# Kernel optimization log

Hardware: AMD Instinct MI355X
Metric: run time of the kernel (lower is better)

The kernel has to match this reference:

```python
import jax, jax.numpy as jnp
import numpy as np

SCALES = (4, 8, 8)
PAD = 2
TOTAL = 256  # prod(SCALES) == frame shift
INDENT = PAD * TOTAL
BN_EPS = 1e-3  # keras BatchNormalization default


def _bn(x, g, b, m, v):
    return (x - m) * jax.lax.rsqrt(v + BN_EPS) * g + b


def _conv1d_valid(x, w):
    # x: [B, T, Cin], w: [K, Cin, Cout]
    return jax.lax.conv_general_dilated(x, w, (1,), 'VALID',
                                         dimension_numbers=('NWC', 'WIO', 'NWC'))


def _mel_conv_same(x, w):
    # per-mel-bin shared 1D conv along time. x: [B, T, M], w: [K]
    B, T, M = x.shape
    lhs = x.transpose(0, 2, 1).reshape(B * M, T, 1)
    rhs = w.reshape(-1, 1, 1)
    y = jax.lax.conv_general_dilated(lhs, rhs, (1,), 'SAME',
                                     dimension_numbers=('NWC', 'WIO', 'NWC'))
    return y.reshape(B, M, T).transpose(0, 2, 1)


def _gru(x, Wx, Wh, bx, bh):
    # keras GRUCell (reset_after=True): gate order z, r, h; h' = z*h + (1-z)*hh
    xp = x @ Wx + bx  # [B, T, 3H], input projection hoisted out of the scan
    H = Wh.shape[0]
    h0 = jnp.zeros((x.shape[0], H), x.dtype)

    def step(h, xt):
        rp = h @ Wh + bh
        xz, xr, xh = jnp.split(xt, 3, axis=-1)
        rz, rr, rh = jnp.split(rp, 3, axis=-1)
        z = jax.nn.sigmoid(xz + rz)
        r = jax.nn.sigmoid(xr + rr)
        hh = jnp.tanh(xh + r * rh)
        hn = z * h + (1.0 - z) * hh
        return hn, hn

    _, ys = jax.lax.scan(step, h0, xp.transpose(1, 0, 2))
    return ys.transpose(1, 0, 2)


def setup_inputs() -> dict:
    key = jax.random.key(0)
    ks = iter(jax.random.split(key, 64))
    B, T_MEL, M, C, H, R = 4, 44, 80, 128, 512, 10
    T_UP = TOTAL * (T_MEL - 2 * PAD)  # 10240
    s = 0.05
    d = {}
    d['audios'] = jax.random.normal(next(ks), (B, T_UP + 1), jnp.float32)
    d['mels'] = jax.random.normal(next(ks), (B, T_MEL, M), jnp.float32)
    d['w_mel0'] = jnp.full((2 * SCALES[0] + 1,), 1.0 / (2 * SCALES[0] + 1), jnp.float32)
    d['w_mel1'] = jnp.full((2 * SCALES[1] + 1,), 1.0 / (2 * SCALES[1] + 1), jnp.float32)
    d['w_mel2'] = jnp.full((2 * SCALES[2] + 1,), 1.0 / (2 * SCALES[2] + 1), jnp.float32)
    d['mr_conv0_w'] = jax.random.normal(next(ks), (5, M, C), jnp.float32) * s
    d['mr_bn0_g'] = jax.random.uniform(next(ks), (C,), jnp.float32, 0.5, 1.5)
    d['mr_bn0_b'] = jax.random.normal(next(ks), (C,), jnp.float32) * s
    d['mr_bn0_m'] = jnp.zeros((C,), jnp.float32)
    d['mr_bn0_v'] = jnp.ones((C,), jnp.float32)
    d['r_w1'] = jax.random.normal(next(ks), (R, C, C), jnp.float32) * s
    d['r_bn1_g'] = jax.random.uniform(next(ks), (R, C), jnp.float32, 0.5, 1.5)
    d['r_bn1_b'] = jax.random.normal(next(ks), (R, C), jnp.float32) * s
    d['r_bn1_m'] = jnp.zeros((R, C), jnp.float32)
    d['r_bn1_v'] = jnp.ones((R, C), jnp.float32)
    d['r_w2'] = jax.random.normal(next(ks), (R, C, C), jnp.float32) * s
    d['r_bn2_g'] = jax.random.uniform(next(ks), (R, C), jnp.float32, 0.5, 1.5)
    d['r_bn2_b'] = jax.random.normal(next(ks), (R, C), jnp.float32) * s
    d['r_bn2_m'] = jnp.zeros((R, C), jnp.float32)
    d['r_bn2_v'] = jnp.ones((R, C), jnp.float32)
    d['mr_out_w'] = jax.random.normal(next(ks), (C, C), jnp.float32) * s
    d['mr_out_b'] = jnp.zeros((C,), jnp.float32)
    A4 = C // 4  # 32
    d['Wi'] = jax.random.normal(next(ks), (1 + M + A4, H), jnp.float32) * s
    d['bi'] = jnp.zeros((H,), jnp.float32)
    d['Wx0'] = jax.random.normal(next(ks), (H, 3 * H), jnp.float32) * s
    d['Wh0'] = jax.random.normal(next(ks), (H, 3 * H), jnp.float32) * s
    d['bx0'] = jnp.zeros((3 * H,), jnp.float32)
    d['bh0'] = jnp.zeros((3 * H,), jnp.float32)
    d['Wx1'] = jax.random.normal(next(ks), (H + A4, 3 * H), jnp.float32) * s
    d['Wh1'] = jax.random.normal(next(ks), (H, 3 * H), jnp.float32) * s
    d['bx1'] = jnp.zeros((3 * H,), jnp.float32)
    d['bh1'] = jnp.zeros((3 * H,), jnp.float32)
    d['Wd0'] = jax.random.normal(next(ks), (H + A4, H), jnp.float32) * s
    d['bd0'] = jnp.zeros((H,), jnp.float32)
    d['Wd1'] = jax.random.normal(next(ks), (H + A4, H), jnp.float32) * s
    d['bd1'] = jnp.zeros((H,), jnp.float32)
    d['Wp'] = jax.random.normal(next(ks), (H, 30), jnp.float32) * s
    d['bp'] = jnp.zeros((30,), jnp.float32)
    return d


def reference(audios, mels, w_mel0, w_mel1, w_mel2,
              mr_conv0_w, mr_bn0_g, mr_bn0_b, mr_bn0_m, mr_bn0_v,
              r_w1, r_bn1_g, r_bn1_b, r_bn1_m, r_bn1_v,
              r_w2, r_bn2_g, r_bn2_b, r_bn2_m, r_bn2_v,
              mr_out_w, mr_out_b, Wi, bi,
              Wx0, Wh0, bx0, bh0, Wx1, Wh1, bx1, bh1,
              Wd0, bd0, Wd1, bd1, Wp, bp):
    # ---- UpsampleNet mel branch: nearest upsample + smoothing conv per scale ----
    x = mels
    for w, scale in zip((w_mel0, w_mel1, w_mel2), SCALES):
        x = jnp.repeat(x, scale, axis=1)
        x = _mel_conv_same(x, w)
    mels_up = x[:, INDENT:-INDENT, :]  # [B, T_up, 80]

    # ---- UpsampleNet aux branch: MelResNet (inference BN) + nearest upsample ----
    a = jax.nn.relu(_bn(_conv1d_valid(mels, mr_conv0_w),
                        mr_bn0_g, mr_bn0_b, mr_bn0_m, mr_bn0_v))
    for i in range(r_w1.shape[0]):
        y = jax.nn.relu(_bn(a @ r_w1[i], r_bn1_g[i], r_bn1_b[i], r_bn1_m[i], r_bn1_v[i]))
        y = _bn(y @ r_w2[i], r_bn2_g[i], r_bn2_b[i], r_bn2_m[i], r_bn2_v[i])
        a = a + y
    a = a @ mr_out_w + mr_out_b
    aux = jnp.repeat(a, TOTAL, axis=1)  # [B, T_up, 128]
    a0, a1, a2, a3 = jnp.split(aux, 4, axis=-1)

    # ---- WaveRNN teacher-forced trunk ----
    x = jnp.concatenate([audios[:, :-1, None], mels_up, a0], axis=-1)
    x = x @ Wi + bi  # [B, T_up, 512]
    x = _gru(x, Wx0, Wh0, bx0, bh0) + x
    x = _gru(jnp.concatenate([x, a1], axis=-1), Wx1, Wh1, bx1, bh1) + x
    x = jax.nn.relu(jnp.concatenate([x, a2], axis=-1) @ Wd0 + bd0) + x
    x = jax.nn.relu(jnp.concatenate([x, a3], axis=-1) @ Wd1 + bd1) + x
    logits = x @ Wp + bp  # [B, T_up, 30] (MoL parameters)
    return logits
```

## Files before the change

### kernel.cpp

```cpp
#include <hip/hip_runtime.h>
#include <hip/hip_bf16.h>

#define T_SEQ 10240
#define GRU_W 8

typedef short bf16x8 __attribute__((ext_vector_type(8)));
typedef float f32x4 __attribute__((ext_vector_type(4)));

__device__ __forceinline__ float bf2f(unsigned short u) {
    return __uint_as_float(((unsigned int)u) << 16);
}

__global__ void upsample_kernel(const float* __restrict__ in, float* __restrict__ out,
                                const float* __restrict__ wk,
                                int B, int Tin, int Tout, int shift, int taps)
{
    int idx = blockIdx.x * blockDim.x + threadIdx.x;
    int total = B * Tout * 80;
    if (idx >= total) return;
    int m = idx % 80;
    int r = idx / 80;
    int t = r % Tout;
    int b = r / Tout;
    int s = taps >> 1;
    float acc = 0.f;
    for (int d = -s; d <= s; ++d) {
        int i = t + d;
        if (i >= 0 && i < Tout)
            acc += in[((size_t)b * Tin + (i >> shift)) * 80 + m] * wk[d + s];
    }
    out[idx] = acc;
}

__global__ __launch_bounds__(128) void conv0_kernel(
    const float* __restrict__ mels, const float* __restrict__ w,
    const float* __restrict__ g, const float* __restrict__ b,
    const float* __restrict__ m_, const float* __restrict__ v_,
    float* __restrict__ a)
{
    __shared__ float xin[400];
    int bt = blockIdx.x;
    int bb = bt / 40, t = bt % 40;
    int c = threadIdx.x;
    for (int idx = c; idx < 400; idx += 128)
        xin[idx] = mels[((size_t)bb * 44 + t + idx / 80) * 80 + (idx % 80)];
    __syncthreads();
    float s = 0.f;
    for (int q = 0; q < 400; ++q) s += xin[q] * w[q * 128 + c];
    s = (s - m_[c]) * rsqrtf(v_[c] + 1e-3f) * g[c] + b[c];
    a[bt * 128 + c] = fmaxf(s, 0.f);
}

__global__ __launch_bounds__(128) void resblock_kernel(
    const float* __restrict__ W1, const float* __restrict__ W2,
    const float* __restrict__ g1, const float* __restrict__ b1,
    const float* __restrict__ m1, const float* __restrict__ v1,
    const float* __restrict__ g2, const float* __restrict__ b2,
    const float* __restrict__ m2, const float* __restrict__ v2,
    float* __restrict__ a)
{
    __shared__ float ain[128], y1[128];
    int tok = blockIdx.x;
    int c = threadIdx.x;
    ain[c] = a[tok * 128 + c];
    __syncthreads();
    float s = 0.f;
    #pragma unroll 8
    for (int k = 0; k < 128; ++k) s += ain[k] * W1[k * 128 + c];
    s = (s - m1[c]) * rsqrtf(v1[c] + 1e-3f) * g1[c] + b1[c];
    y1[c] = fmaxf(s, 0.f);
    __syncthreads();
    float s2 = 0.f;
    #pragma unroll 8
    for (int k = 0; k < 128; ++k) s2 += y1[k] * W2[k * 128 + c];
    s2 = (s2 - m2[c]) * rsqrtf(v2[c] + 1e-3f) * g2[c] + b2[c];
    a[tok * 128 + c] = ain[c] + s2;
}

__global__ __launch_bounds__(128) void outmat_kernel(
    const float* __restrict__ W, const float* __restrict__ bias,
    const float* __restrict__ a, float* __restrict__ out)
{
    __shared__ float ain[128];
    int tok = blockIdx.x;
    int c = threadIdx.x;
    ain[c] = a[tok * 128 + c];
    __syncthreads();
    float s = 0.f;
    #pragma unroll 8
    for (int k = 0; k < 128; ++k) s += ain[k] * W[k * 128 + c];
    out[tok * 128 + c] = s + bias[c];
}

__device__ __forceinline__ float fetchA(int mode, int row, int k, int K,
    const float* audio, const float* melsup, const float* cond, const float* xA)
{
    if (k >= K) return 0.f;
    int b = row / T_SEQ;
    int t = row - b * T_SEQ;
    if (mode == 0) {
        if (k == 0) return audio[(size_t)b * (T_SEQ + 1) + t];
        if (k < 81) return melsup[((size_t)b * 11264 + 512 + t) * 80 + (k - 1)];
        return cond[((size_t)b * 40 + (t >> 8)) * 128 + (k - 81)];
    }
    if (k < 512) return xA[(size_t)row * 512 + k];
    int co = (mode == 2) ? 32 : (mode == 3) ? 64 : 96;
    return cond[((size_t)b * 40 + (t >> 8)) * 128 + co + (k - 512)];
}

__global__ __launch_bounds__(256) void gemm_big(
    int mode, int N, int K,
    const float* __restrict__ W, const float* __restrict__ bias1,
    const float* __restrict__ bias2,
    const float* __restrict__ audio, const float* __restrict__ melsup,
    const float* __restrict__ cond, const float* __restrict__ xA,
    const float* __restrict__ resid, float* __restrict__ outF,
    __hip_bfloat16* __restrict__ outB)
{
    __shared__ float As[16][68];
    __shared__ float Bs[16][68];
    const int tid = threadIdx.x;
    const int row0 = blockIdx.y * 64;
    const int col0 = blockIdx.x * 64;
    const int tx = tid & 15, ty = tid >> 4;
    float acc[4][4] = {};
    const int nkt = (K + 15) >> 4;
    for (int kt = 0; kt < nkt; ++kt) {
        const int kb = kt << 4;
        #pragma unroll
        for (int l = 0; l < 4; ++l) {
            int k = (tid >> 6) + l * 4;
            int m = tid & 63;
            float bv = 0.f;
            if (kb + k < K) bv = W[(size_t)(kb + k) * N + col0 + m];
            Bs[k][m] = bv;
        }
        if (mode != 0) {
            int m = tid >> 2, kq = tid & 3;
            int row = row0 + m;
            int k = kb + kq * 4;
            if (k + 3 < 512) {
                float4 v = *reinterpret_cast<const float4*>(xA + (size_t)row * 512 + k);
                As[kq * 4 + 0][m] = v.x; As[kq * 4 + 1][m] = v.y;
                As[kq * 4 + 2][m] = v.z; As[kq * 4 + 3][m] = v.w;
            } else {
                #pragma unroll
                for (int i = 0; i < 4; ++i)
                    As[kq * 4 + i][m] = fetchA(mode, row, k + i, K, audio, melsup, cond, xA);
            }
        } else {
            #pragma unroll
            for (int l = 0; l < 4; ++l) {
                int k = (tid >> 6) + l * 4;
                int m = tid & 63;
                As[k][m] = fetchA(0, row0 + m, kb + k, K, audio, melsup, cond, xA);
            }
        }
        __syncthreads();
        #pragma unroll
        for (int k = 0; k < 16; ++k) {
            float a0 = As[k][(ty << 2) + 0], a1 = As[k][(ty << 2) + 1];
            float a2 = As[k][(ty << 2) + 2], a3 = As[k][(ty << 2) + 3];
            float b0 = Bs[k][(tx << 2) + 0], b1 = Bs[k][(tx << 2) + 1];
            float b2 = Bs[k][(tx << 2) + 2], b3 = Bs[k][(tx << 2) + 3];
            acc[0][0] += a0 * b0; acc[0][1] += a0 * b1; acc[0][2] += a0 * b2; acc[0][3] += a0 * b3;
            acc[1][0] += a1 * b0; acc[1][1] += a1 * b1; acc[1][2] += a1 * b2; acc[1][3] += a1 * b3;
            acc[2][0] += a2 * b0; acc[2][1] += a2 * b1; acc[2][2] += a2 * b2; acc[2][3] += a2 * b3;
            acc[3][0] += a3 * b0; acc[3][1] += a3 * b1; acc[3][2] += a3 * b2; acc[3][3] += a3 * b3;
        }
        __syncthreads();
    }
    #pragma unroll
    for (int i = 0; i < 4; ++i) {
        int row = row0 + (ty << 2) + i;
        #pragma unroll
        for (int jt = 0; jt < 4; ++jt) {
            int col = col0 + (tx << 2) + jt;
            float v = acc[i][jt] + bias1[col];
            if (bias2 && col < 1024) v += bias2[col];
            if (mode == 0) {
                outF[(size_t)row * N + col] = v;
            } else if (mode <= 2) {
                outB[(size_t)row * 1536 + col] = __float2bfloat16(v);
            } else {
                v = fmaxf(v, 0.f) + resid[(size_t)row * 512 + col];
                outF[(size_t)row * 512 + col] = v;
            }
        }
    }
}

__global__ __launch_bounds__(256) void pack_wh_kernel(const float* __restrict__ Wh,
                                                      unsigned short* __restrict__ out)
{
    int gid = blockIdx.x * 256 + threadIdx.x;
    int l = gid & 63;
    int idx = gid >> 6;
    int kt = idx & 15; idx >>= 4;
    int ntL = idx & 1; idx >>= 1;
    int w = idx % 6;
    int wg = idx / 6;
    int nt = 2 * w + ntL;
    int g = nt >> 2, u = nt & 3;
    int n = g * 512 + wg * 64 + u * 16 + (l & 15);
    int k0 = kt * 32 + (l >> 4) * 8;
    unsigned short* dst = out + (size_t)gid * 8;
    #pragma unroll
    for (int i = 0; i < 8; ++i) {
        __hip_bfloat16 hv = __float2bfloat16(Wh[(size_t)(k0 + i) * 1536 + n]);
        dst[i] = *reinterpret_cast<unsigned short*>(&hv);
    }
}

__global__ __launch_bounds__(512, 2) void gru_mfma8(
    const unsigned short* __restrict__ wpack,
    const float* __restrict__ bh,
    const __hip_bfloat16* __restrict__ xp,
    float* __restrict__ xio,
    unsigned int* __restrict__ hpair,
    int T)
{
    __shared__ alignas(16) unsigned short h_sh[16 * 512];
    __shared__ alignas(16) unsigned short xp_sh[2][4][3][64];
    __shared__ alignas(8)  float xv_sh[2][4][64];
    __shared__ alignas(16) float acc_sh[12][16][4];

    const int tid = threadIdx.x;
    const int wg = blockIdx.x;
    const int w = tid >> 6;
    const int l = tid & 63;

    {
        uint4* z = reinterpret_cast<uint4*>(h_sh);
        z[tid] = make_uint4(0, 0, 0, 0);
        z[tid + 512] = make_uint4(0, 0, 0, 0);
    }

    bf16x8 wf[2][16];
    if (w < 6) {
        const bf16x8* wp = reinterpret_cast<const bf16x8*>(wpack);
        const int base = (wg * 6 + w) * 2 * 16 * 64;
        #pragma unroll
        for (int n = 0; n < 2; ++n)
            #pragma unroll
            for (int kt = 0; kt < 16; ++kt)
                wf[n][kt] = wp[base + (n * 16 + kt) * 64 + l];
    }

    float bhh = 0.f, hprev = 0.f;
    if (tid < 256) bhh = bh[1024 + wg * 64 + (tid & 63)];

    if (tid < 128) {
        for (int z = tid; z < 192; z += 128) {
            int bg = z >> 4, s = z & 15;
            int b = bg / 3, g = bg % 3;
            unsigned long long v = *reinterpret_cast<const unsigned long long*>(
                reinterpret_cast<const unsigned short*>(xp) +
                (size_t)(b * T) * 1536 + g * 512 + wg * 64 + s * 4);
            *reinterpret_cast<unsigned long long*>(&xp_sh[0][b][g][s * 4]) = v;
        }
        int b = tid >> 5, pr = tid & 31;
        float2 v = *reinterpret_cast<const float2*>(
            xio + (size_t)(b * T) * 512 + wg * 64 + pr * 2);
        *reinterpret_cast<float2*>(&xv_sh[0][b][pr * 2]) = v;
    }
    __syncthreads();

    const unsigned long long* hp64 = reinterpret_cast<const unsigned long long*>(hpair);

    for (int t = 0; t < T; ++t) {
        const int cur = t & 1, nxt = cur ^ 1;

        const unsigned long long* src = hp64 + (size_t)cur * 1024 + tid * 2;
        const unsigned tg = (unsigned)t & 0xffffu;
        unsigned long long u0 = __hip_atomic_load(src + 0, __ATOMIC_RELAXED, __HIP_MEMORY_SCOPE_AGENT);
        unsigned long long u1 = __hip_atomic_load(src + 1, __ATOMIC_RELAXED, __HIP_MEMORY_SCOPE_AGENT);
        while ((((unsigned)(u0 >> 16) & 0xffffu) != tg) | ((unsigned)(u0 >> 48) != tg) |
               (((unsigned)(u1 >> 16) & 0xffffu) != tg) | ((unsigned)(u1 >> 48) != tg)) {
            __builtin_amdgcn_s_sleep(1);
            u0 = __hip_atomic_load(src + 0, __ATOMIC_RELAXED, __HIP_MEMORY_SCOPE_AGENT);
            u1 = __hip_atomic_load(src + 1, __ATOMIC_RELAXED, __HIP_MEMORY_SCOPE_AGENT);
        }
        {
            const int pb = tid >> 7;
            const int j0 = (tid * 4) & 511;
            unsigned long long wv =
                (u0 & 0xffffull) | ((u0 >> 32) & 0xffffull) << 16 |
                (u1 & 0xffffull) << 32 | ((u1 >> 32) & 0xffffull) << 48;
            const int chunk = (j0 >> 3) ^ (pb & 7);
            *reinterpret_cast<unsigned long long*>(
                reinterpret_cast<char*>(h_sh) + pb * 1024 + chunk * 16 + (j0 & 7) * 2) = wv;
        }
        __syncthreads();

        if (w >= 6 && t + 1 < T) {
            int t6 = tid - 384;
            for (int z = t6; z < 192; z += 128) {
                int bg = z >> 4, s = z & 15;
                int b = bg / 3, g = bg % 3;
                unsigned long long v = *reinterpret_cast<const unsigned long long*>(
                    reinterpret_cast<const unsigned short*>(xp) +
                    (size_t)(b * T + t + 1) * 1536 + g * 512 + wg * 64 + s * 4);
                *reinterpret_cast<unsigned long long*>(&xp_sh[nxt][b][g][s * 4]) = v;
            }
            int b = t6 >> 5, pr = t6 & 31;
            float2 v = *reinterpret_cast<const float2*>(
                xio + (size_t)(b * T + t + 1) * 512 + wg * 64 + pr * 2);
            *reinterpret_cast<float2*>(&xv_sh[nxt][b][pr * 2]) = v;
        }

        if (w < 6) {
            f32x4 acc0 = {0, 0, 0, 0}, acc1 = {0, 0, 0, 0};
            const int rb = l & 15, q = l >> 4;
            #pragma unroll
            for (int kt = 0; kt < 16; ++kt) {
                bf16x8 afr = *reinterpret_cast<const bf16x8*>(
                    reinterpret_cast<const char*>(h_sh) + rb * 1024 +
                    ((((kt * 4 + q) ^ (rb & 7))) << 4));
                acc0 = __builtin_amdgcn_mfma_f32_16x16x32_bf16(afr, wf[0][kt], acc0, 0, 0, 0);
                acc1 = __builtin_amdgcn_mfma_f32_16x16x32_bf16(afr, wf[1][kt], acc1, 0, 0, 0);
            }
            if (l < 16) {
                *reinterpret_cast<f32x4*>(&acc_sh[2 * w][l][0]) = acc0;
                *reinterpret_cast<f32x4*>(&acc_sh[2 * w + 1][l][0]) = acc1;
            }
        }
        __syncthreads();

        if (tid < 256) {
            const int b = tid >> 6, jl = tid & 63, j = wg * 64 + jl;
            const int u = jl >> 4, n16 = jl & 15;
            float az = acc_sh[u][n16][b];
            float ar = acc_sh[4 + u][n16][b];
            float ah = acc_sh[8 + u][n16][b];
            float xz = bf2f(xp_sh[cur][b][0][jl]);
            float xr = bf2f(xp_sh[cur][b][1][jl]);
            float xh = bf2f(xp_sh[cur][b][2][jl]);
            float xv = xv_sh[cur][b][jl];
            float z = 1.f / (1.f + __expf(-(xz + az)));
            float r = 1.f / (1.f + __expf(-(xr + ar)));
            float e2 = __expf(-2.f * (xh + r * (ah + bhh)));
            float hh = (1.f - e2) / (1.f + e2);
            float hn = z * hprev + (1.f - z) * hh;
            hprev = hn;
            __hip_bfloat16 hb16 = __float2bfloat16(hn);
            unsigned hv = ((unsigned)((t + 1) & 0xffff) << 16) |
                          (unsigned)*reinterpret_cast<unsigned short*>(&hb16);
            __hip_atomic_store(hpair + (size_t)nxt * 2048 + b * 512 + j, hv,
                               __ATOMIC_RELAXED, __HIP_MEMORY_SCOPE_AGENT);
            xio[(size_t)(b * T + t) * 512 + j] = xv + hn;
        }
    }
}

__global__ __launch_bounds__(256) void wp_kernel(
    const float* __restrict__ x, const float* __restrict__ Wp,
    const float* __restrict__ bp, float* __restrict__ out)
{
    int r = threadIdx.x >> 5, c = threadIdx.x & 31;
    size_t row = (size_t)blockIdx.x * 8 + r;
    if (c >= 30) return;
    const float* xr = x + row * 512;
    float acc = 0.f;
    #pragma unroll 8
    for (int k = 0; k < 512; ++k) acc += xr[k] * Wp[k * 30 + c];
    out[row * 30 + c] = acc + bp[c];
}

extern "C" void kernel_launch(void* const* d_in, const int* in_sizes, int n_in,
                              void* d_out, int out_size, void* d_ws, size_t ws_size,
                              hipStream_t stream)
{
    const float* audios = (const float*)d_in[0];
    const float* mels   = (const float*)d_in[1];
    const float* w_mel0 = (const float*)d_in[2];
    const float* w_mel1 = (const float*)d_in[3];
    const float* w_mel2 = (const float*)d_in[4];
    const float* conv0w = (const float*)d_in[5];
    const float* bn0g = (const float*)d_in[6];
    const float* bn0b = (const float*)d_in[7];
    const float* bn0m = (const float*)d_in[8];
    const float* bn0v = (const float*)d_in[9];
    const float* r_w1   = (const float*)d_in[10];
    const float* r_bn1g = (const float*)d_in[11];
    const float* r_bn1b = (const float*)d_in[12];
    const float* r_bn1m = (const float*)d_in[13];
    const float* r_bn1v = (const float*)d_in[14];
    const float* r_w2   = (const float*)d_in[15];
    const float* r_bn2g = (const float*)d_in[16];
    const float* r_bn2b = (const float*)d_in[17];
    const float* r_bn2m = (const float*)d_in[18];
    const float* r_bn2v = (const float*)d_in[19];
    const float* mr_out_w = (const float*)d_in[20];
    const float* mr_out_b = (const float*)d_in[21];
    const float* Wi = (const float*)d_in[22];
    const float* bi = (const float*)d_in[23];
    const float* Wx0 = (const float*)d_in[24];
    const float* Wh0 = (const float*)d_in[25];
    const float* bx0 = (const float*)d_in[26];
    const float* bh0 = (const float*)d_in[27];
    const float* Wx1 = (const float*)d_in[28];
    const float* Wh1 = (const float*)d_in[29];
    const float* bx1 = (const float*)d_in[30];
    const float* bh1 = (const float*)d_in[31];
    const float* Wd0 = (const float*)d_in[32];
    const float* bd0 = (const float*)d_in[33];
    const float* Wd1 = (const float*)d_in[34];
    const float* bd1 = (const float*)d_in[35];
    const float* Wp = (const float*)d_in[36];
    const float* bp = (const float*)d_in[37];

    char* ws = (char*)d_ws;
    size_t off = 0;
    auto alloc = [&](size_t n) { size_t r = off; off += (n + 255) & ~(size_t)255; return r; };
    const size_t M = 4 * (size_t)T_SEQ;
    size_t xp_off = alloc(M * 1536 * 2);
    size_t x_off  = alloc(M * 512 * 4);
    size_t s1_off = alloc((size_t)4 * 176 * 80 * 4);
    size_t s2_off = alloc((size_t)4 * 1408 * 80 * 4);
    size_t s3_off = alloc((size_t)4 * 11264 * 80 * 4);
    size_t ca_off = alloc((size_t)160 * 128 * 4);
    size_t cf_off = alloc((size_t)160 * 128 * 4);
    size_t wp0_off = alloc((size_t)98304 * 8 * 2);
    size_t wp1_off = alloc((size_t)98304 * 8 * 2);
    size_t hp_off  = alloc(2 * 2048 * 4);

    __hip_bfloat16* xp = (__hip_bfloat16*)(ws + xp_off);
    float* x3   = (float*)(ws + xp_off);
    float* xbuf = (float*)(ws + x_off);
    float* st1  = (float*)(ws + s1_off);
    float* st2  = (float*)(ws + s2_off);
    float* st3  = (float*)(ws + s3_off);
    float* conda = (float*)(ws + ca_off);
    float* condf = (float*)(ws + cf_off);
    unsigned short* wpack0 = (unsigned short*)(ws + wp0_off);
    unsigned short* wpack1 = (unsigned short*)(ws + wp1_off);
    unsigned int* hpair = (unsigned int*)(ws + hp_off);
    float* outp = (float*)d_out;

    pack_wh_kernel<<<384, 256, 0, stream>>>(Wh0, wpack0);
    pack_wh_kernel<<<384, 256, 0, stream>>>(Wh1, wpack1);

    {
        int tot1 = 4 * 176 * 80;
        upsample_kernel<<<(tot1 + 255) / 256, 256, 0, stream>>>(mels, st1, w_mel0, 4, 44, 176, 2, 9);
        int tot2 = 4 * 1408 * 80;
        upsample_kernel<<<(tot2 + 255) / 256, 256, 0, stream>>>(st1, st2, w_mel1, 4, 176, 1408, 3, 17);
        int tot3 = 4 * 11264 * 80;
        upsample_kernel<<<(tot3 + 255) / 256, 256, 0, stream>>>(st2, st3, w_mel2, 4, 1408, 11264, 3, 17);
    }
    conv0_kernel<<<160, 128, 0, stream>>>(mels, conv0w, bn0g, bn0b, bn0m, bn0v, conda);
    for (int i = 0; i < 10; ++i) {
        resblock_kernel<<<160, 128, 0, stream>>>(
            r_w1 + (size_t)i * 128 * 128, r_w2 + (size_t)i * 128 * 128,
            r_bn1g + i * 128, r_bn1b + i * 128, r_bn1m + i * 128, r_bn1v + i * 128,
            r_bn2g + i * 128, r_bn2b + i * 128, r_bn2m + i * 128, r_bn2v + i * 128,
            conda);
    }
    outmat_kernel<<<160, 128, 0, stream>>>(mr_out_w, mr_out_b, conda, condf);

    dim3 blk(256);
    gemm_big<<<dim3(8, 640), blk, 0, stream>>>(0, 512, 113, Wi, bi, nullptr,
        audios, st3, condf, nullptr, nullptr, xbuf, nullptr);
    gemm_big<<<dim3(24, 640), blk, 0, stream>>>(1, 1536, 512, Wx0, bx0, bh0,
        nullptr, nullptr, condf, xbuf, nullptr, nullptr, xp);
    hipMemsetAsync(ws + hp_off, 0, 2 * 2048 * 4, stream);
    gru_mfma8<<<GRU_W, 512, 0, stream>>>(wpack0, bh0, xp, xbuf, hpair, T_SEQ);
    gemm_big<<<dim3(24, 640), blk, 0, stream>>>(2, 1536, 544, Wx1, bx1, bh1,
        nullptr, nullptr, condf, xbuf, nullptr, nullptr, xp);
    hipMemsetAsync(ws + hp_off, 0, 2 * 2048 * 4, stream);
    gru_mfma8<<<GRU_W, 512, 0, stream>>>(wpack1, bh1, xp, xbuf, hpair, T_SEQ);
    gemm_big<<<dim3(8, 640), blk, 0, stream>>>(3, 512, 544, Wd0, bd0, nullptr,
        nullptr, nullptr, condf, xbuf, xbuf, x3, nullptr);
    gemm_big<<<dim3(8, 640), blk, 0, stream>>>(4, 512, 544, Wd1, bd1, nullptr,
        nullptr, nullptr, condf, x3, x3, xbuf, nullptr);
    wp_kernel<<<5120, 256, 0, stream>>>(xbuf, Wp, bp, outp);
}
```

Measured before the change: 47.59 ms.

## Restructure GRU recurrence to 4 waves each owning all three gates per column

Each block now runs 4 waves of 256 threads instead of 8, and each wave holds Wh fragments for the z, r and h gates of its 16 columns, packed in a new order. The gate nonlinearity is computed directly from MFMA accumulator registers, which removes the acc_sh shared buffer and one __syncthreads per timestep. The h buffer in shared memory is double-buffered. Next-step xp and x inputs are prefetched into registers by the computing lanes rather than staged through shared memory by spare waves. The aim is a shorter serial critical path per step, at the cost of more registers per wave and fewer waves to hide latency.

Result: no change. 48.35 ms (+1.6%).

```diff
diff --git a/kernel.cpp b/kernel.cpp
--- a/kernel.cpp
+++ b/kernel.cpp
@@ -197,12 +197,10 @@
     int l = gid & 63;
     int idx = gid >> 6;
     int kt = idx & 15; idx >>= 4;
-    int ntL = idx & 1; idx >>= 1;
-    int w = idx % 6;
-    int wg = idx / 6;
-    int nt = 2 * w + ntL;
-    int g = nt >> 2, u = nt & 3;
-    int n = g * 512 + wg * 64 + u * 16 + (l & 15);
+    int g = idx % 3;
+    int ww = idx / 3;
+    int wg = ww >> 2, w = ww & 3;
+    int n = g * 512 + wg * 64 + w * 16 + (l & 15);
     int k0 = kt * 32 + (l >> 4) * 8;
     unsigned short* dst = out + (size_t)gid * 8;
     #pragma unroll
@@ -212,7 +210,7 @@
     }
 }
 
-__global__ __launch_bounds__(512, 2) void gru_mfma8(
+__global__ __launch_bounds__(256, 1) void gru_mfma8(
     const unsigned short* __restrict__ wpack,
     const float* __restrict__ bh,
     const __hip_bfloat16* __restrict__ xp,
@@ -220,135 +218,126 @@
     unsigned int* __restrict__ hpair,
     int T)
 {
-    __shared__ alignas(16) unsigned short h_sh[16 * 512];
-    __shared__ alignas(16) unsigned short xp_sh[2][4][3][64];
-    __shared__ alignas(8)  float xv_sh[2][4][64];
-    __shared__ alignas(16) float acc_sh[12][16][4];
+    __shared__ alignas(16) unsigned short h_sh[2][16 * 512];
 
     const int tid = threadIdx.x;
     const int wg = blockIdx.x;
     const int w = tid >> 6;
     const int l = tid & 63;
 
+    bf16x8 wf[3][16];
     {
-        uint4* z = reinterpret_cast<uint4*>(h_sh);
-        z[tid] = make_uint4(0, 0, 0, 0);
-        z[tid + 512] = make_uint4(0, 0, 0, 0);
-    }
-
-    bf16x8 wf[2][16];
-    if (w < 6) {
         const bf16x8* wp = reinterpret_cast<const bf16x8*>(wpack);
-        const int base = (wg * 6 + w) * 2 * 16 * 64;
-        #pragma unroll
-        for (int n = 0; n < 2; ++n)
+        const int wbase = (wg * 4 + w) * 3 * 1024;
+        #pragma unroll
+        for (int g = 0; g < 3; ++g)
             #pragma unroll
             for (int kt = 0; kt < 16; ++kt)
-                wf[n][kt] = wp[base + (n * 16 + kt) * 64 + l];
-    }
-
-    float bhh = 0.f, hprev = 0.f;
-    if (tid < 256) bhh = bh[1024 + wg * 64 + (tid & 63)];
-
-    if (tid < 128) {
-        for (int z = tid; z < 192; z += 128) {
-            int bg = z >> 4, s = z & 15;
-            int b = bg / 3, g = bg % 3;
-            unsigned long long v = *reinterpret_cast<const unsigned long long*>(
-                reinterpret_cast<const unsigned short*>(xp) +
-                (size_t)(b * T) * 1536 + g * 512 + wg * 64 + s * 4);
-            *reinterpret_cast<unsigned long long*>(&xp_sh[0][b][g][s * 4]) = v;
-        }
-        int b = tid >> 5, pr = tid & 31;
-        float2 v = *reinterpret_cast<const float2*>(
-            xio + (size_t)(b * T) * 512 + wg * 64 + pr * 2);
-        *reinterpret_cast<float2*>(&xv_sh[0][b][pr * 2]) = v;
+                wf[g][kt] = wp[wbase + (g * 16 + kt) * 64 + l];
+    }
+
+    {
+        uint4* z = reinterpret_cast<uint4*>(&h_sh[0][0]);
+        #pragma unroll
+        for (int i = 0; i < 8; ++i) z[tid + 256 * i] = make_uint4(0, 0, 0, 0);
+    }
+
+    const int j = wg * 64 + w * 16 + (l & 15);
+    const float bhh = bh[1024 + j];
+    float hprev[4] = {0.f, 0.f, 0.f, 0.f};
+    float xz_c[4], xr_c[4], xh_c[4], xv_c[4];
+    if (l < 16) {
+        #pragma unroll
+        for (int b = 0; b < 4; ++b) {
+            const size_t rb = (size_t)b * T;
+            xz_c[b] = bf2f(*reinterpret_cast<const unsigned short*>(xp + rb * 1536 + j));
+            xr_c[b] = bf2f(*reinterpret_cast<const unsigned short*>(xp + rb * 1536 + 512 + j));
+            xh_c[b] = bf2f(*reinterpret_cast<const unsigned short*>(xp + rb * 1536 + 1024 + j));
+            xv_c[b] = xio[rb * 512 + j];
+        }
     }
     __syncthreads();
 
     const unsigned long long* hp64 = reinterpret_cast<const unsigned long long*>(hpair);
+    const int pb = tid >> 6;
+    const int pchunk = (tid & 63) ^ (pb & 7);
 
     for (int t = 0; t < T; ++t) {
         const int cur = t & 1, nxt = cur ^ 1;
 
-        const unsigned long long* src = hp64 + (size_t)cur * 1024 + tid * 2;
+        const unsigned long long* src = hp64 + (size_t)cur * 1024 + tid * 4;
         const unsigned tg = (unsigned)t & 0xffffu;
         unsigned long long u0 = __hip_atomic_load(src + 0, __ATOMIC_RELAXED, __HIP_MEMORY_SCOPE_AGENT);
         unsigned long long u1 = __hip_atomic_load(src + 1, __ATOMIC_RELAXED, __HIP_MEMORY_SCOPE_AGENT);
+        unsigned long long u2 = __hip_atomic_load(src + 2, __ATOMIC_RELAXED, __HIP_MEMORY_SCOPE_AGENT);
+        unsigned long long u3 = __hip_atomic_load(src + 3, __ATOMIC_RELAXED, __HIP_MEMORY_SCOPE_AGENT);
         while ((((unsigned)(u0 >> 16) & 0xffffu) != tg) | ((unsigned)(u0 >> 48) != tg) |
-               (((unsigned)(u1 >> 16) & 0xffffu) != tg) | ((unsigned)(u1 >> 48) != tg)) {
+               (((unsigned)(u1 >> 16) & 0xffffu) != tg) | ((unsigned)(u1 >> 48) != tg) |
+               (((unsigned)(u2 >> 16) & 0xffffu) != tg) | ((unsigned)(u2 >> 48) != tg) |
+               (((unsigned)(u3 >> 16) & 0xffffu) != tg) | ((unsigned)(u3 >> 48) != tg)) {
             __builtin_amdgcn_s_sleep(1);
             u0 = __hip_atomic_load(src + 0, __ATOMIC_RELAXED, __HIP_MEMORY_SCOPE_AGENT);
             u1 = __hip_atomic_load(src + 1, __ATOMIC_RELAXED, __HIP_MEMORY_SCOPE_AGENT);
+            u2 = __hip_atomic_load(src + 2, __ATOMIC_RELAXED, __HIP_MEMORY_SCOPE_AGENT);
+            u3 = __hip_atomic_load(src + 3, __ATOMIC_RELAXED, __HIP_MEMORY_SCOPE_AGENT);
         }
         {
-            const int pb = tid >> 7;
-            const int j0 = (tid * 4) & 511;
-            unsigned long long wv =
-                (u0 & 0xffffull) | ((u0 >> 32) & 0xffffull) << 16 |
-                (u1 & 0xffffull) << 32 | ((u1 >> 32) & 0xffffull) << 48;
-            const int chunk = (j0 >> 3) ^ (pb & 7);
-            *reinterpret_cast<unsigned long long*>(
-                reinterpret_cast<char*>(h_sh) + pb * 1024 + chunk * 16 + (j0 & 7) * 2) = wv;
+            uint4 wv;
+            wv.x = (unsigned)(u0 & 0xffffull) | ((unsigned)((u0 >> 32) & 0xffffull) << 16);
+            wv.y = (unsigned)(u1 & 0xffffull) | ((unsigned)((u1 >> 32) & 0xffffull) << 16);
+            wv.z = (unsigned)(u2 & 0xffffull) | ((unsigned)((u2 >> 32) & 0xffffull) << 16);
+            wv.w = (unsigned)(u3 & 0xffffull) | ((unsigned)((u3 >> 32) & 0xffffull) << 16);
+            *reinterpret_cast<uint4*>(
+                reinterpret_cast<char*>(&h_sh[cur][0]) + pb * 1024 + pchunk * 16) = wv;
         }
         __syncthreads();
 
-        if (w >= 6 && t + 1 < T) {
-            int t6 = tid - 384;
-            for (int z = t6; z < 192; z += 128) {
-                int bg = z >> 4, s = z & 15;
-                int b = bg / 3, g = bg % 3;
-                unsigned long long v = *reinterpret_cast<const unsigned long long*>(
-                    reinterpret_cast<const unsigned short*>(xp) +
-                    (size_t)(b * T + t + 1) * 1536 + g * 512 + wg * 64 + s * 4);
-                *reinterpret_cast<unsigned long long*>(&xp_sh[nxt][b][g][s * 4]) = v;
-            }
-            int b = t6 >> 5, pr = t6 & 31;
-            float2 v = *reinterpret_cast<const float2*>(
-                xio + (size_t)(b * T + t + 1) * 512 + wg * 64 + pr * 2);
-            *reinterpret_cast<float2*>(&xv_sh[nxt][b][pr * 2]) = v;
-        }
-
-        if (w < 6) {
-            f32x4 acc0 = {0, 0, 0, 0}, acc1 = {0, 0, 0, 0};
-            const int rb = l & 15, q = l >> 4;
+        f32x4 acc0 = {0, 0, 0, 0}, acc1 = {0, 0, 0, 0}, acc2 = {0, 0, 0, 0};
+        const int rb = l & 15, q = l >> 4;
+        const char* hb = reinterpret_cast<const char*>(&h_sh[cur][0]);
+        #pragma unroll
+        for (int kt = 0; kt < 16; ++kt) {
+            bf16x8 afr = *reinterpret_cast<const bf16x8*>(
+                hb + rb * 1024 + ((((kt * 4 + q) ^ (rb & 7))) << 4));
+            acc0 = __builtin_amdgcn_mfma_f32_16x16x32_bf16(afr, wf[0][kt], acc0, 0, 0, 0);
+            acc1 = __builtin_amdgcn_mfma_f32_16x16x32_bf16(afr, wf[1][kt], acc1, 0, 0, 0);
+            acc2 = __builtin_amdgcn_mfma_f32_16x16x32_bf16(afr, wf[2][kt], acc2, 0, 0, 0);
+        }
+
+        if (l < 16) {
+            float hn[4];
             #pragma unroll
-            for (int kt = 0; kt < 16; ++kt) {
-                bf16x8 afr = *reinterpret_cast<const bf16x8*>(
-                    reinterpret_cast<const char*>(h_sh) + rb * 1024 +
-                    ((((kt * 4 + q) ^ (rb & 7))) << 4));
-                acc0 = __builtin_amdgcn_mfma_f32_16x16x32_bf16(afr, wf[0][kt], acc0, 0, 0, 0);
-                acc1 = __builtin_amdgcn_mfma_f32_16x16x32_bf16(afr, wf[1][kt], acc1, 0, 0, 0);
-            }
-            if (l < 16) {
-                *reinterpret_cast<f32x4*>(&acc_sh[2 * w][l][0]) = acc0;
-                *reinterpret_cast<f32x4*>(&acc_sh[2 * w + 1][l][0]) = acc1;
-            }
-        }
-        __syncthreads();
-
-        if (tid < 256) {
-            const int b = tid >> 6, jl = tid & 63, j = wg * 64 + jl;
-            const int u = jl >> 4, n16 = jl & 15;
-            float az = acc_sh[u][n16][b];
-            float ar = acc_sh[4 + u][n16][b];
-            float ah = acc_sh[8 + u][n16][b];
-            float xz = bf2f(xp_sh[cur][b][0][jl]);
-            float xr = bf2f(xp_sh[cur][b][1][jl]);
-            float xh = bf2f(xp_sh[cur][b][2][jl]);
-            float xv = xv_sh[cur][b][jl];
-            float z = 1.f / (1.f + __expf(-(xz + az)));
-            float r = 1.f / (1.f + __expf(-(xr + ar)));
-            float e2 = __expf(-2.f * (xh + r * (ah + bhh)));
-            float hh = (1.f - e2) / (1.f + e2);
-            float hn = z * hprev + (1.f - z) * hh;
-            hprev = hn;
-            __hip_bfloat16 hb16 = __float2bfloat16(hn);
-            unsigned hv = ((unsigned)((t + 1) & 0xffff) << 16) |
-                          (unsigned)*reinterpret_cast<unsigned short*>(&hb16);
-            __hip_atomic_store(hpair + (size_t)nxt * 2048 + b * 512 + j, hv,
-                               __ATOMIC_RELAXED, __HIP_MEMORY_SCOPE_AGENT);
-            xio[(size_t)(b * T + t) * 512 + j] = xv + hn;
+            for (int b = 0; b < 4; ++b) {
+                float z = 1.f / (1.f + __expf(-(xz_c[b] + acc0[b])));
+                float r = 1.f / (1.f + __expf(-(xr_c[b] + acc1[b])));
+                float e2 = __expf(-2.f * (xh_c[b] + r * (acc2[b] + bhh)));
+                float hh = (1.f - e2) / (1.f + e2);
+                hn[b] = z * hprev[b] + (1.f - z) * hh;
+                hprev[b] = hn[b];
+            }
+            if (t + 1 < T) {
+                const unsigned ptag = (unsigned)((t + 1) & 0xffff) << 16;
+                #pragma unroll
+                for (int b = 0; b < 4; ++b) {
+                    __hip_bfloat16 hb16 = __float2bfloat16(hn[b]);
+                    __hip_atomic_store(hpair + (size_t)nxt * 2048 + b * 512 + j,
+                                       ptag | (unsigned)*reinterpret_cast<unsigned short*>(&hb16),
+                                       __ATOMIC_RELAXED, __HIP_MEMORY_SCOPE_AGENT);
+                }
+            }
+            #pragma unroll
+            for (int b = 0; b < 4; ++b)
+                xio[((size_t)b * T + t) * 512 + j] = xv_c[b] + hn[b];
+            if (t + 1 < T) {
+                #pragma unroll
+                for (int b = 0; b < 4; ++b) {
+                    const size_t rb2 = (size_t)b * T + t + 1;
+                    xz_c[b] = bf2f(*reinterpret_cast<const unsigned short*>(xp + rb2 * 1536 + j));
+                    xr_c[b] = bf2f(*reinterpret_cast<const unsigned short*>(xp + rb2 * 1536 + 512 + j));
+                    xh_c[b] = bf2f(*reinterpret_cast<const unsigned short*>(xp + rb2 * 1536 + 1024 + j));
+                    xv_c[b] = xio[rb2 * 512 + j];
+                }
+            }
         }
     }
 }
@@ -465,11 +454,11 @@
     gemm_big<<<dim3(24, 640), blk, 0, stream>>>(1, 1536, 512, Wx0, bx0, bh0,
         nullptr, nullptr, condf, xbuf, nullptr, nullptr, xp);
     hipMemsetAsync(ws + hp_off, 0, 2 * 2048 * 4, stream);
-    gru_mfma8<<<GRU_W, 512, 0, stream>>>(wpack0, bh0, xp, xbuf, hpair, T_SEQ);
+    gru_mfma8<<<GRU_W, 256, 0, stream>>>(wpack0, bh0, xp, xbuf, hpair, T_SEQ);
     gemm_big<<<dim3(24, 640), blk, 0, stream>>>(2, 1536, 544, Wx1, bx1, bh1,
         nullptr, nullptr, condf, xbuf, nullptr, nullptr, xp);
     hipMemsetAsync(ws + hp_off, 0, 2 * 2048 * 4, stream);
-    gru_mfma8<<<GRU_W, 512, 0, stream>>>(wpack1, bh1, xp, xbuf, hpair, T_SEQ);
+    gru_mfma8<<<GRU_W, 256, 0, stream>>>(wpack1, bh1, xp, xbuf, hpair, T_SEQ);
     gemm_big<<<dim3(8, 640), blk, 0, stream>>>(3, 512, 544, Wd0, bd0, nullptr,
         nullptr, nullptr, condf, xbuf, xbuf, x3, nullptr);
     gemm_big<<<dim3(8, 640), blk, 0, stream>>>(4, 512, 544, Wd1, bd1, nullptr,
```
